# Kernel tuning notes

Measured on AMD Instinct MI355X. Metric: run time of the kernel, lower is better.

Reference implementation:

```python
import jax, jax.numpy as jnp
import numpy as np

N = 100000
E = 1000000
IN_C, HID, OUT_C = 128, 128, 40
DROPOUT_P = 0.5
BN_EPS = 1e-5


def setup_inputs() -> dict:
    key = jax.random.key(0)
    ks = jax.random.split(key, 10)
    x = jax.random.normal(ks[0], (N, IN_C), dtype=jnp.float32)
    edge_index = jax.random.randint(ks[1], (2, E), 0, N, dtype=jnp.int32)

    def glorot(k, fan_in, fan_out):
        lim = np.sqrt(6.0 / (fan_in + fan_out)).astype(np.float32)
        return jax.random.uniform(k, (fan_in, fan_out), jnp.float32, -lim, lim)

    return {
        "x": x,
        "edge_index": edge_index,
        "W1": glorot(ks[2], IN_C, HID), "b1": jnp.zeros((HID,), jnp.float32),
        "g1": jnp.ones((HID,), jnp.float32), "be1": jnp.zeros((HID,), jnp.float32),
        "W2": glorot(ks[3], HID, HID), "b2": jnp.zeros((HID,), jnp.float32),
        "g2": jnp.ones((HID,), jnp.float32), "be2": jnp.zeros((HID,), jnp.float32),
        "W3": glorot(ks[4], HID, OUT_C), "b3": jnp.zeros((OUT_C,), jnp.float32),
    }


def _deg_inv_sqrt(dst):
    # degree from destination nodes, +1 for the added self loop (PyG gcn_norm)
    deg = jax.ops.segment_sum(jnp.ones((E,), jnp.float32), dst, num_segments=N) + 1.0
    return jax.lax.rsqrt(deg)


def _gcn_conv(h, W, b, src, dst, dinv):
    # h: [N, Cin] -> [N, Cout]; y = D^-1/2 (A + I) D^-1/2 (h W) + b
    hw = h @ W
    norm = dinv[src] * dinv[dst]                      # [E]
    msg = hw[src] * norm[:, None]                     # [E, Cout] gather (memory-bound)
    agg = jax.ops.segment_sum(msg, dst, num_segments=N)
    agg = agg + hw * (dinv * dinv)[:, None]           # self-loop contribution
    return agg + b


def _batchnorm(h, gamma, beta):
    mu = jnp.mean(h, axis=0)
    var = jnp.mean(jnp.square(h - mu), axis=0)        # biased, training mode
    return (h - mu) * jax.lax.rsqrt(var + BN_EPS) * gamma + beta


def _dropout(h, key):
    keep = jax.random.bernoulli(key, 1.0 - DROPOUT_P, h.shape)
    return jnp.where(keep, h / (1.0 - DROPOUT_P), 0.0)


def reference(x, edge_index, W1, b1, g1, be1, W2, b2, g2, be2, W3, b3):
    src, dst = edge_index[0], edge_index[1]
    dinv = _deg_inv_sqrt(dst)
    dk = jax.random.split(jax.random.key(42), 2)

    h = _gcn_conv(x, W1, b1, src, dst, dinv)
    h = _dropout(jax.nn.relu(_batchnorm(h, g1, be1)), dk[0])

    h = _gcn_conv(h, W2, b2, src, dst, dinv)
    h = _dropout(jax.nn.relu(_batchnorm(h, g2, be2)), dk[1])

    h = _gcn_conv(h, W3, b3, src, dst, dinv)
    return jax.nn.log_softmax(h, axis=1)
```

## Files before the change

### kernel.cpp

```cpp
#include <hip/hip_runtime.h>
#include <math.h>

typedef __attribute__((ext_vector_type(8))) short bf16x8;
typedef __attribute__((ext_vector_type(4))) float f32x4;

__device__ __forceinline__ float bfbits2f(unsigned short b){
  return __uint_as_float(((unsigned)b) << 16);
}
__device__ __forceinline__ unsigned short f2bfbits(float f){
  unsigned u = __float_as_uint(f);
  unsigned r = u + 0x7fffu + ((u >> 16) & 1u);
  return (unsigned short)(r >> 16);
}

__device__ __forceinline__ uint4 ld16(const void* __restrict__ base, unsigned byteoff){
  return *(const uint4*)((const char*)base + byteoff);
}
__device__ __forceinline__ uint2 ld8(const void* __restrict__ base, unsigned byteoff){
  return *(const uint2*)((const char*)base + byteoff);
}

__host__ __device__ __forceinline__ unsigned rotl32(unsigned v, int d){
  return (v << d) | (v >> (32 - d));
}
__host__ __device__ __forceinline__ void tf2x32(unsigned k0, unsigned k1,
                                                unsigned c0, unsigned c1,
                                                unsigned &o0, unsigned &o1)
{
  unsigned ks2 = k0 ^ k1 ^ 0x1BD11BDAu;
  unsigned x0 = c0 + k0, x1 = c1 + k1;
#define TFR(r) x0 += x1; x1 = rotl32(x1, r); x1 ^= x0;
  TFR(13) TFR(15) TFR(26) TFR(6)
  x0 += k1;  x1 += ks2 + 1u;
  TFR(17) TFR(29) TFR(16) TFR(24)
  x0 += ks2; x1 += k0 + 2u;
  TFR(13) TFR(15) TFR(26) TFR(6)
  x0 += k0;  x1 += k1 + 3u;
  TFR(17) TFR(29) TFR(16) TFR(24)
  x0 += k1;  x1 += ks2 + 4u;
  TFR(13) TFR(15) TFR(26) TFR(6)
  x0 += ks2; x1 += k0 + 5u;
#undef TFR
  o0 = x0; o1 = x1;
}

__device__ __forceinline__ void gen_mask(unsigned* __restrict__ mask,
                                         unsigned mk0, unsigned mk1,
                                         int g, int total, int M)
{
  for (int wi = g; wi < M; wi += total){
    unsigned bits = 0u;
    #pragma unroll 4
    for (int j = 0; j < 32; j++){
      unsigned w0, w1;
      tf2x32(mk0, mk1, 0u, (unsigned)wi * 32u + (unsigned)j, w0, w1);
      bits |= (((w0 ^ w1) >> 31) << j);
    }
    mask[wi] = bits;
  }
}

__global__ __launch_bounds__(256) void k_countpos(const int* __restrict__ dst,
                                                  int* __restrict__ cnt,
                                                  int* __restrict__ pos, int E,
                                                  unsigned* __restrict__ mask,
                                                  unsigned mk0, unsigned mk1, int M)
{
  int g = blockIdx.x * 256 + threadIdx.x;
  int base = g * 4;
  if (base + 3 < E){
    int4 d = ((const int4*)dst)[g];
    int4 p;
    p.x = atomicAdd(&cnt[d.x], 1);
    p.y = atomicAdd(&cnt[d.y], 1);
    p.z = atomicAdd(&cnt[d.z], 1);
    p.w = atomicAdd(&cnt[d.w], 1);
    gen_mask(mask, mk0, mk1, g, gridDim.x * 256, M);
    ((int4*)pos)[g] = p;
  } else {
    for (int j = 0; j < 4; j++){
      int e = base + j;
      if (e < E) pos[e] = atomicAdd(&cnt[dst[e]], 1);
    }
    gen_mask(mask, mk0, mk1, g, gridDim.x * 256, M);
  }
}

__global__ __launch_bounds__(256) void k_blocksum(const int* __restrict__ cnt,
                                                  int* __restrict__ bsum, int N)
{
  __shared__ int sh[256];
  int t = threadIdx.x;
  int base = blockIdx.x * 1024 + t * 4;
  int s = 0;
  #pragma unroll
  for (int j = 0; j < 4; j++){ int i = base + j; if (i < N) s += cnt[i]; }
  sh[t] = s; __syncthreads();
  for (int off = 128; off; off >>= 1){
    if (t < off) sh[t] += sh[t + off];
    __syncthreads();
  }
  if (t == 0) bsum[blockIdx.x] = sh[0];
}

__global__ __launch_bounds__(256) void k_scansums(const int* __restrict__ bsum,
                                                  int* __restrict__ boff,
                                                  int* __restrict__ rowstart,
                                                  int NB, int N)
{
  __shared__ int sh[256];
  int t = threadIdx.x;
  int v = (t < NB) ? bsum[t] : 0;
  sh[t] = v; __syncthreads();
  for (int off = 1; off < 256; off <<= 1){
    int x = sh[t];
    int y = (t >= off) ? sh[t - off] : 0;
    __syncthreads();
    sh[t] = x + y;
    __syncthreads();
  }
  if (t < NB) boff[t] = sh[t] - v;
  if (t == NB - 1) rowstart[N] = sh[t];
}

__global__ __launch_bounds__(256) void k_scanfinal(const int* __restrict__ cnt,
                                                   const int* __restrict__ boff,
                                                   int* __restrict__ rowstart,
                                                   float* __restrict__ dinv, int N)
{
  __shared__ int sh[256];
  int t = threadIdx.x;
  int base = blockIdx.x * 1024 + t * 4;
  int c0 = 0, c1 = 0, c2 = 0, c3 = 0;
  if (base + 0 < N) c0 = cnt[base + 0];
  if (base + 1 < N) c1 = cnt[base + 1];
  if (base + 2 < N) c2 = cnt[base + 2];
  if (base + 3 < N) c3 = cnt[base + 3];
  int s = c0 + c1 + c2 + c3;
  sh[t] = s; __syncthreads();
  for (int off = 1; off < 256; off <<= 1){
    int x = sh[t];
    int y = (t >= off) ? sh[t - off] : 0;
    __syncthreads();
    sh[t] = x + y;
    __syncthreads();
  }
  int excl = sh[t] - s + boff[blockIdx.x];
  if (base + 0 < N){ rowstart[base+0] = excl;          dinv[base+0] = rsqrtf((float)c0 + 1.f); }
  if (base + 1 < N){ rowstart[base+1] = excl+c0;       dinv[base+1] = rsqrtf((float)c1 + 1.f); }
  if (base + 2 < N){ rowstart[base+2] = excl+c0+c1;    dinv[base+2] = rsqrtf((float)c2 + 1.f); }
  if (base + 3 < N){ rowstart[base+3] = excl+c0+c1+c2; dinv[base+3] = rsqrtf((float)c3 + 1.f); }
}

__global__ __launch_bounds__(256) void k_fill(const int* __restrict__ src,
                                              const int* __restrict__ dst,
                                              const int* __restrict__ pos,
                                              const int* __restrict__ rowstart,
                                              int* __restrict__ csr, int E,
                                              unsigned* __restrict__ mask,
                                              unsigned mk0, unsigned mk1, int M)
{
  int g = blockIdx.x * 256 + threadIdx.x;
  int base = g * 4;
  if (base + 3 < E){
    int4 d = ((const int4*)dst)[g];
    int4 p = ((const int4*)pos)[g];
    int4 s = ((const int4*)src)[g];
    int r0 = rowstart[d.x], r1 = rowstart[d.y], r2 = rowstart[d.z], r3 = rowstart[d.w];
    csr[r0 + p.x] = s.x;
    csr[r1 + p.y] = s.y;
    csr[r2 + p.z] = s.z;
    csr[r3 + p.w] = s.w;
  } else {
    for (int j = 0; j < 4; j++){
      int e = base + j;
      if (e < E) csr[rowstart[dst[e]] + pos[e]] = src[e];
    }
  }
  gen_mask(mask, mk0, mk1, g, gridDim.x * 256, M);
}

__global__ __launch_bounds__(256) void k_wt(const float* __restrict__ W1,
                                            const float* __restrict__ W2,
                                            const float* __restrict__ W3,
                                            unsigned short* __restrict__ WT1,
                                            unsigned short* __restrict__ WT2,
                                            unsigned short* __restrict__ WT3)
{
  const float* W; unsigned short* WT; int Cout, Cpad;
  if (blockIdx.x == 0){ W = W1; WT = WT1; Cout = 128; Cpad = 128; }
  else if (blockIdx.x == 1){ W = W2; WT = WT2; Cout = 128; Cpad = 128; }
  else { W = W3; WT = WT3; Cout = 40; Cpad = 48; }
  int tot = Cpad * 128;
  for (int i = threadIdx.x; i < tot; i += 256){
    int n = i >> 7, k = i & 127;
    float v = (n < Cout) ? W[k * Cout + n] : 0.f;
    WT[i] = f2bfbits(v);
  }
}

template<int NT, int MODE>
__global__ __launch_bounds__(256) void k_gemm_mfma(const void* __restrict__ Ap,
                                                   const unsigned short* __restrict__ WT,
                                                   const float* __restrict__ dinv,
                                                   const float* __restrict__ stats,
                                                   const float* __restrict__ g,
                                                   const float* __restrict__ be,
                                                   const unsigned* __restrict__ mask,
                                                   float invN,
                                                   unsigned short* __restrict__ outb,
                                                   int N, int Cout, int Cstride)
{
  __shared__ uint4 Wl4[NT * 16 * 16];
  __shared__ uint4 Al4[64 * 16];
  __shared__ float bnS[128], bnB[128];
  const int t = threadIdx.x;
  const int w = t >> 6, l = t & 63;
  const long rb0 = (long)blockIdx.x * 64;
  const int wrow0 = w * 16;

  uint4 rawU[4];
  float4 rawF[4][2];
  unsigned mword[4];
  int rr[4], cc[4];
  bool inr[4];
  #pragma unroll
  for (int i = 0; i < 4; i++){
    int idx = i * 64 + l;
    int r = idx >> 4, c = idx & 15;
    long grow = rb0 + wrow0 + r;
    rr[i] = r; cc[i] = c; inr[i] = (grow < N);
    if (inr[i]){
      if (MODE == 0){
        const float* ap = (const float*)Ap + grow * 128 + c * 8;
        rawF[i][0] = *(const float4*)ap;
        rawF[i][1] = *(const float4*)(ap + 4);
      } else {
        rawU[i] = *(const uint4*)((const unsigned short*)Ap + grow * 128 + c * 8);
        mword[i] = mask[((unsigned)grow << 2) + (c >> 2)];
      }
    }
  }

  {
    const uint4* s4 = (const uint4*)WT;
    const int tot = NT * 16 * 16;
    for (int i = t; i < tot; i += 256){
      int n = i >> 4, c = i & 15;
      Wl4[n * 16 + (c ^ (n & 15))] = s4[i];
    }
  }
  if (MODE == 2 && t < 128){
    float ss = 0.f, qq = 0.f;
    #pragma unroll
    for (int i = 0; i < 16; i++){
      ss += stats[i * 256 + t];
      qq += stats[i * 256 + 128 + t];
    }
    float mean = ss * invN;
    float var = fmaxf(qq * invN - mean * mean, 0.f);
    float rstd = rsqrtf(var + 1e-5f);
    float sc = g[t] * rstd;
    bnS[t] = sc;
    bnB[t] = be[t] - mean * sc;
  }
  __syncthreads();

  #pragma unroll
  for (int i = 0; i < 4; i++){
    uint4 chunk = make_uint4(0u, 0u, 0u, 0u);
    if (inr[i]){
      if (MODE == 0){
        chunk.x = (unsigned)f2bfbits(rawF[i][0].x) | ((unsigned)f2bfbits(rawF[i][0].y) << 16);
        chunk.y = (unsigned)f2bfbits(rawF[i][0].z) | ((unsigned)f2bfbits(rawF[i][0].w) << 16);
        chunk.z = (unsigned)f2bfbits(rawF[i][1].x) | ((unsigned)f2bfbits(rawF[i][1].y) << 16);
        chunk.w = (unsigned)f2bfbits(rawF[i][1].z) | ((unsigned)f2bfbits(rawF[i][1].w) << 16);
      } else {
        unsigned mb = mword[i] >> ((cc[i] & 3) * 8);
        const unsigned* rw = &rawU[i].x;
        unsigned* cw = &chunk.x;
        #pragma unroll
        for (int h = 0; h < 4; h++){
          int ch = cc[i] * 8 + 2 * h;
          float f0 = bfbits2f((unsigned short)(rw[h] & 0xffffu));
          float f1 = bfbits2f((unsigned short)(rw[h] >> 16));
          f0 = fmaxf(fmaf(f0, bnS[ch],     bnB[ch]),     0.f);
          f1 = fmaxf(fmaf(f1, bnS[ch + 1], bnB[ch + 1]), 0.f);
          f0 = ((mb >> (2 * h))     & 1u) ? 0.f : f0 * 2.f;
          f1 = ((mb >> (2 * h + 1)) & 1u) ? 0.f : f1 * 2.f;
          cw[h] = (unsigned)f2bfbits(f0) | ((unsigned)f2bfbits(f1) << 16);
        }
      }
    }
    Al4[(wrow0 + rr[i]) * 16 + (cc[i] ^ rr[i])] = chunk;
  }

  const int lm = l & 15, q = l >> 4;

  f32x4 acc[NT];
  #pragma unroll
  for (int nt = 0; nt < NT; nt++){
    acc[nt][0] = 0.f; acc[nt][1] = 0.f; acc[nt][2] = 0.f; acc[nt][3] = 0.f;
  }

  #pragma unroll
  for (int kt = 0; kt < 4; kt++){
    const int x = kt * 4 + q;
    bf16x8 a = *(const bf16x8*)&Al4[(wrow0 + lm) * 16 + (x ^ lm)];
    #pragma unroll
    for (int nt = 0; nt < NT; nt++){
      int brow = nt * 16 + lm;
      bf16x8 b = *(const bf16x8*)&Wl4[brow * 16 + (x ^ (brow & 15))];
      acc[nt] = __builtin_amdgcn_mfma_f32_16x16x32_bf16(a, b, acc[nt], 0, 0, 0);
    }
  }

  #pragma unroll
  for (int r = 0; r < 4; r++){
    long row = rb0 + wrow0 + q * 4 + r;
    if (row < N){
      float dv = dinv[row];
      #pragma unroll
      for (int nt = 0; nt < NT; nt++){
        int col = nt * 16 + lm;
        if (col < Cout)
          outb[row * Cstride + col] = f2bfbits(acc[nt][r] * dv);
      }
    }
  }
}

#define ACC8(U) do{ uint4 _u = (U); \
  a0 += bfbits2f((unsigned short)(_u.x & 0xffffu)); \
  a1 += bfbits2f((unsigned short)(_u.x >> 16)); \
  a2 += bfbits2f((unsigned short)(_u.y & 0xffffu)); \
  a3 += bfbits2f((unsigned short)(_u.y >> 16)); \
  a4 += bfbits2f((unsigned short)(_u.z & 0xffffu)); \
  a5 += bfbits2f((unsigned short)(_u.z >> 16)); \
  a6 += bfbits2f((unsigned short)(_u.w & 0xffffu)); \
  a7 += bfbits2f((unsigned short)(_u.w >> 16)); }while(0)

__global__ __launch_bounds__(256) void k_agg128s(const unsigned short* __restrict__ hw,
                                                 const int* __restrict__ rs,
                                                 const int* __restrict__ csr,
                                                 const float* __restrict__ dinv,
                                                 unsigned short* __restrict__ outb,
                                                 float* __restrict__ stats,
                                                 int N)
{
  const int l = threadIdx.x;
  const int ns = l >> 4;
  const int sl = l & 15;
  const int ty = threadIdx.y;
  const int grp = ty * 4 + ns;
  const int base = blockIdx.x * 32;
  const unsigned slB = (unsigned)sl * 16u;

  float s0=0.f,s1=0.f,s2=0.f,s3=0.f,s4=0.f,s5=0.f,s6=0.f,s7=0.f;
  float q0=0.f,q1=0.f,q2=0.f,q3=0.f,q4=0.f,q5=0.f,q6=0.f,q7=0.f;

  #pragma unroll 1
  for (int it = 0; it < 2; it++){
    int v = base + it * 16 + grp;
    if (v < N){
      float a0=0.f,a1=0.f,a2=0.f,a3=0.f,a4=0.f,a5=0.f,a6=0.f,a7=0.f;
      ACC8(ld16(hw, (unsigned)v * 256u + slB));
      int e0 = rs[v], e1 = rs[v + 1];
      int i = e0;
      for (; i + 4 <= e1; i += 4){
        int sa = csr[i], sb = csr[i+1], sc = csr[i+2], sd = csr[i+3];
        uint4 m0 = ld16(hw, (unsigned)sa * 256u + slB);
        uint4 m1 = ld16(hw, (unsigned)sb * 256u + slB);
        uint4 m2 = ld16(hw, (unsigned)sc * 256u + slB);
        uint4 m3 = ld16(hw, (unsigned)sd * 256u + slB);
        ACC8(m0); ACC8(m1); ACC8(m2); ACC8(m3);
      }
      for (; i < e1; i++){
        ACC8(ld16(hw, (unsigned)csr[i] * 256u + slB));
      }
      float dv = dinv[v];
      a0*=dv; a1*=dv; a2*=dv; a3*=dv; a4*=dv; a5*=dv; a6*=dv; a7*=dv;
      uint4 o;
      o.x = (unsigned)f2bfbits(a0) | ((unsigned)f2bfbits(a1) << 16);
      o.y = (unsigned)f2bfbits(a2) | ((unsigned)f2bfbits(a3) << 16);
      o.z = (unsigned)f2bfbits(a4) | ((unsigned)f2bfbits(a5) << 16);
      o.w = (unsigned)f2bfbits(a6) | ((unsigned)f2bfbits(a7) << 16);
      *(uint4*)((char*)outb + (unsigned)v * 256u + slB) = o;
      s0+=a0; q0=fmaf(a0,a0,q0);  s1+=a1; q1=fmaf(a1,a1,q1);
      s2+=a2; q2=fmaf(a2,a2,q2);  s3+=a3; q3=fmaf(a3,a3,q3);
      s4+=a4; q4=fmaf(a4,a4,q4);  s5+=a5; q5=fmaf(a5,a5,q5);
      s6+=a6; q6=fmaf(a6,a6,q6);  s7+=a7; q7=fmaf(a7,a7,q7);
    }
  }

  __shared__ float shS[16][128], shQ[16][128];
  *(float4*)&shS[grp][sl * 8]     = make_float4(s0, s1, s2, s3);
  *(float4*)&shS[grp][sl * 8 + 4] = make_float4(s4, s5, s6, s7);
  *(float4*)&shQ[grp][sl * 8]     = make_float4(q0, q1, q2, q3);
  *(float4*)&shQ[grp][sl * 8 + 4] = make_float4(q4, q5, q6, q7);
  __syncthreads();
  int t = ty * 64 + threadIdx.x;
  if (t < 128){
    float ss = 0.f, qq = 0.f;
    #pragma unroll
    for (int g2 = 0; g2 < 16; g2++){ ss += shS[g2][t]; qq += shQ[g2][t]; }
    float* dstat = stats + (blockIdx.x & 15) * 256;
    atomicAdd(&dstat[t], ss);
    atomicAdd(&dstat[128 + t], qq);
  }
}

__global__ __launch_bounds__(256) void k_agg40lsm(const unsigned short* __restrict__ hw,
                                                  const int* __restrict__ rs,
                                                  const int* __restrict__ csr,
                                                  const float* __restrict__ dinv,
                                                  const float* __restrict__ b3,
                                                  float* __restrict__ out, int N)
{
  const int l = threadIdx.x;
  const int ns = l >> 4, sl = l & 15;
  const int v = blockIdx.x * 16 + threadIdx.y * 4 + ns;
  const bool act = (v < N) && (sl < 10);
  const unsigned slB = (unsigned)sl * 8u;
  float a0 = 0.f, a1 = 0.f, a2 = 0.f, a3 = 0.f, dv = 1.f;
  if (act){
    dv = dinv[v];
    uint2 u = ld8(hw, (unsigned)v * 128u + slB);
    a0 = bfbits2f((unsigned short)(u.x & 0xffffu));
    a1 = bfbits2f((unsigned short)(u.x >> 16));
    a2 = bfbits2f((unsigned short)(u.y & 0xffffu));
    a3 = bfbits2f((unsigned short)(u.y >> 16));
    int e0 = rs[v], e1 = rs[v + 1];
    int i = e0;
#define ACCU2(U) do{ uint2 _u = (U); \
    a0 += bfbits2f((unsigned short)(_u.x & 0xffffu)); \
    a1 += bfbits2f((unsigned short)(_u.x >> 16)); \
    a2 += bfbits2f((unsigned short)(_u.y & 0xffffu)); \
    a3 += bfbits2f((unsigned short)(_u.y >> 16)); }while(0)
    for (; i + 4 <= e1; i += 4){
      int sa = csr[i], sb = csr[i+1], sc = csr[i+2], sd = csr[i+3];
      uint2 m0 = ld8(hw, (unsigned)sa * 128u + slB);
      uint2 m1 = ld8(hw, (unsigned)sb * 128u + slB);
      uint2 m2 = ld8(hw, (unsigned)sc * 128u + slB);
      uint2 m3 = ld8(hw, (unsigned)sd * 128u + slB);
      ACCU2(m0); ACCU2(m1); ACCU2(m2); ACCU2(m3);
    }
    for (; i < e1; i++){
      ACCU2(ld8(hw, (unsigned)csr[i] * 128u + slB));
    }
#undef ACCU2
  }
  float x0 = act ? fmaf(a0, dv, b3[sl * 4 + 0]) : -INFINITY;
  float x1 = act ? fmaf(a1, dv, b3[sl * 4 + 1]) : -INFINITY;
  float x2 = act ? fmaf(a2, dv, b3[sl * 4 + 2]) : -INFINITY;
  float x3 = act ? fmaf(a3, dv, b3[sl * 4 + 3]) : -INFINITY;
  float m = fmaxf(fmaxf(x0, x1), fmaxf(x2, x3));
  #pragma unroll
  for (int off = 8; off; off >>= 1) m = fmaxf(m, __shfl_xor(m, off, 16));
  float e = act ? (expf(x0 - m) + expf(x1 - m) + expf(x2 - m) + expf(x3 - m)) : 0.f;
  #pragma unroll
  for (int off = 8; off; off >>= 1) e += __shfl_xor(e, off, 16);
  float lse = m + logf(e);
  if (act){
    float4 o;
    o.x = x0 - lse; o.y = x1 - lse; o.z = x2 - lse; o.w = x3 - lse;
    *reinterpret_cast<float4*>(out + (size_t)v * 40 + sl * 4) = o;
  }
}

extern "C" void kernel_launch(void* const* d_in, const int* in_sizes, int n_in,
                              void* d_out, int out_size, void* d_ws, size_t ws_size,
                              hipStream_t stream)
{
  const float* x  = (const float*)d_in[0];
  const int* ei   = (const int*)d_in[1];
  const float* W1 = (const float*)d_in[2];
  const float* g1 = (const float*)d_in[4];
  const float* be1= (const float*)d_in[5];
  const float* W2 = (const float*)d_in[6];
  const float* g2 = (const float*)d_in[8];
  const float* be2= (const float*)d_in[9];
  const float* W3 = (const float*)d_in[10];
  const float* b3 = (const float*)d_in[11];
  float* out = (float*)d_out;

  const int N = in_sizes[0] / 128;
  const int E = in_sizes[1] / 2;
  const int* srcv = ei;
  const int* dstv = ei + E;

  char* ws = (char*)d_ws;
  size_t off = 0;
  auto take = [&](size_t bytes) -> void* {
    void* p = ws + off;
    off = (off + bytes + 255) & ~(size_t)255;
    return p;
  };
  int*   cnt      = (int*)  take((size_t)N * 4);
  int*   pos      = (int*)  take((size_t)E * 4);
  int*   rowstart = (int*)  take((size_t)(N + 1) * 4);
  int*   csr      = (int*)  take((size_t)E * 4);
  float* dinv     = (float*)take((size_t)N * 4);
  int*   bsum     = (int*)  take(256 * 4);
  int*   boff     = (int*)  take(256 * 4);
  float* stats1   = (float*)take(2 * 16 * 256 * 4);
  float* stats2   = stats1 + 16 * 256;
  unsigned* mask1 = (unsigned*)take((size_t)N * 4 * 4);
  unsigned* mask2 = (unsigned*)take((size_t)N * 4 * 4);
  unsigned short* WT1 = (unsigned short*)take(128 * 128 * 2);
  unsigned short* WT2 = (unsigned short*)take(128 * 128 * 2);
  unsigned short* WT3 = (unsigned short*)take(48 * 128 * 2);
  unsigned short* bufX = (unsigned short*)take((size_t)N * 128 * 2);
  unsigned short* bufY = (unsigned short*)take((size_t)N * 128 * 2);
  (void)ws_size; (void)n_in; (void)out_size;

  unsigned l1k0, l1k1, l2k0, l2k1;
  tf2x32(0u, 42u, 0u, 0u, l1k0, l1k1);
  tf2x32(0u, 42u, 0u, 1u, l2k0, l2k1);

  const float invN = 1.0f / (float)N;
  const int M = N * 4;
  const int NB = (N + 1023) / 1024;
  dim3 wblk(64, 4);
  dim3 wgrid16((N + 15) / 16);
  dim3 wgrid32((N + 31) / 32);
  const int ggrid = (N + 63) / 64;
  const int egrid = (E + 1023) / 1024;

  hipMemsetAsync(cnt, 0, (size_t)N * 4, stream);
  hipMemsetAsync(stats1, 0, 2 * 16 * 256 * 4, stream);
  k_countpos<<<egrid, 256, 0, stream>>>(dstv, cnt, pos, E, mask1, l1k0, l1k1, M);
  k_blocksum<<<NB, 256, 0, stream>>>(cnt, bsum, N);
  k_scansums<<<1, 256, 0, stream>>>(bsum, boff, rowstart, NB, N);
  k_scanfinal<<<NB, 256, 0, stream>>>(cnt, boff, rowstart, dinv, N);
  k_fill<<<egrid, 256, 0, stream>>>(srcv, dstv, pos, rowstart, csr, E, mask2, l2k0, l2k1, M);
  k_wt<<<3, 256, 0, stream>>>(W1, W2, W3, WT1, WT2, WT3);

  k_gemm_mfma<8, 0><<<ggrid, 256, 0, stream>>>(x, WT1, dinv,
      nullptr, nullptr, nullptr, nullptr, invN, bufX, N, 128, 128);
  k_agg128s<<<wgrid32, wblk, 0, stream>>>(bufX, rowstart, csr, dinv, bufY, stats1, N);

  k_gemm_mfma<8, 2><<<ggrid, 256, 0, stream>>>(bufY, WT2, dinv,
      stats1, g1, be1, mask1, invN, bufX, N, 128, 128);
  k_agg128s<<<wgrid32, wblk, 0, stream>>>(bufX, rowstart, csr, dinv, bufY, stats2, N);

  k_gemm_mfma<3, 2><<<ggrid, 256, 0, stream>>>(bufY, WT3, dinv,
      stats2, g2, be2, mask2, invN, bufX, N, 40, 64);
  k_agg40lsm<<<wgrid16, wblk, 0, stream>>>(bufX, rowstart, csr, dinv, b3, out, N);
}
```

Before: 409.4 us.

## Split dropout mask generation into its own kernel and simplify CSR fill

After: 482.2 us. 1.18x slower.

```diff
diff --git a/kernel.cpp b/kernel.cpp
--- a/kernel.cpp
+++ b/kernel.cpp
@@ -44,45 +44,38 @@
   o0 = x0; o1 = x1;
 }
 
-__device__ __forceinline__ void gen_mask(unsigned* __restrict__ mask,
-                                         unsigned mk0, unsigned mk1,
-                                         int g, int total, int M)
-{
-  for (int wi = g; wi < M; wi += total){
-    unsigned bits = 0u;
-    #pragma unroll 4
-    for (int j = 0; j < 32; j++){
-      unsigned w0, w1;
-      tf2x32(mk0, mk1, 0u, (unsigned)wi * 32u + (unsigned)j, w0, w1);
-      bits |= (((w0 ^ w1) >> 31) << j);
-    }
-    mask[wi] = bits;
-  }
-}
-
-__global__ __launch_bounds__(256) void k_countpos(const int* __restrict__ dst,
-                                                  int* __restrict__ cnt,
-                                                  int* __restrict__ pos, int E,
-                                                  unsigned* __restrict__ mask,
-                                                  unsigned mk0, unsigned mk1, int M)
+__global__ __launch_bounds__(256) void k_mask(unsigned* __restrict__ mask1,
+                                              unsigned* __restrict__ mask2,
+                                              unsigned a0, unsigned a1,
+                                              unsigned b0, unsigned b1, int M)
 {
   int g = blockIdx.x * 256 + threadIdx.x;
-  int base = g * 4;
-  if (base + 3 < E){
-    int4 d = ((const int4*)dst)[g];
-    int4 p;
-    p.x = atomicAdd(&cnt[d.x], 1);
-    p.y = atomicAdd(&cnt[d.y], 1);
-    p.z = atomicAdd(&cnt[d.z], 1);
-    p.w = atomicAdd(&cnt[d.w], 1);
-    gen_mask(mask, mk0, mk1, g, gridDim.x * 256, M);
-    ((int4*)pos)[g] = p;
-  } else {
-    for (int j = 0; j < 4; j++){
-      int e = base + j;
-      if (e < E) pos[e] = atomicAdd(&cnt[dst[e]], 1);
-    }
-    gen_mask(mask, mk0, mk1, g, gridDim.x * 256, M);
+  if (g >= 2 * M) return;
+  const bool second = g >= M;
+  unsigned wi = second ? (unsigned)(g - M) : (unsigned)g;
+  unsigned k0 = second ? b0 : a0;
+  unsigned k1 = second ? b1 : a1;
+  unsigned bits = 0u;
+  #pragma unroll 4
+  for (int j = 0; j < 32; j++){
+    unsigned w0, w1;
+    tf2x32(k0, k1, 0u, wi * 32u + (unsigned)j, w0, w1);
+    bits |= (((w0 ^ w1) >> 31) << j);
+  }
+  (second ? mask2 : mask1)[wi] = bits;
+}
+
+__global__ __launch_bounds__(256) void k_count(const int* __restrict__ dst,
+                                               int* __restrict__ cnt, int E)
+{
+  int g = blockIdx.x * 256 + threadIdx.x;
+  int base = g * 2;
+  if (base + 1 < E){
+    int2 d = ((const int2*)dst)[g];
+    atomicAdd(&cnt[d.x], 1);
+    atomicAdd(&cnt[d.y], 1);
+  } else if (base < E){
+    atomicAdd(&cnt[dst[base]], 1);
   }
 }
 
@@ -123,7 +116,7 @@
   if (t == NB - 1) rowstart[N] = sh[t];
 }
 
-__global__ __launch_bounds__(256) void k_scanfinal(const int* __restrict__ cnt,
+__global__ __launch_bounds__(256) void k_scanfinal(int* __restrict__ cnt,
                                                    const int* __restrict__ boff,
                                                    int* __restrict__ rowstart,
                                                    float* __restrict__ dinv, int N)
@@ -146,38 +139,30 @@
     __syncthreads();
   }
   int excl = sh[t] - s + boff[blockIdx.x];
-  if (base + 0 < N){ rowstart[base+0] = excl;          dinv[base+0] = rsqrtf((float)c0 + 1.f); }
-  if (base + 1 < N){ rowstart[base+1] = excl+c0;       dinv[base+1] = rsqrtf((float)c1 + 1.f); }
-  if (base + 2 < N){ rowstart[base+2] = excl+c0+c1;    dinv[base+2] = rsqrtf((float)c2 + 1.f); }
-  if (base + 3 < N){ rowstart[base+3] = excl+c0+c1+c2; dinv[base+3] = rsqrtf((float)c3 + 1.f); }
+  if (base + 0 < N){ rowstart[base+0] = excl;          cnt[base+0] = excl;          dinv[base+0] = rsqrtf((float)c0 + 1.f); }
+  if (base + 1 < N){ rowstart[base+1] = excl+c0;       cnt[base+1] = excl+c0;       dinv[base+1] = rsqrtf((float)c1 + 1.f); }
+  if (base + 2 < N){ rowstart[base+2] = excl+c0+c1;    cnt[base+2] = excl+c0+c1;    dinv[base+2] = rsqrtf((float)c2 + 1.f); }
+  if (base + 3 < N){ rowstart[base+3] = excl+c0+c1+c2; cnt[base+3] = excl+c0+c1+c2; dinv[base+3] = rsqrtf((float)c3 + 1.f); }
 }
 
 __global__ __launch_bounds__(256) void k_fill(const int* __restrict__ src,
                                               const int* __restrict__ dst,
-                                              const int* __restrict__ pos,
-                                              const int* __restrict__ rowstart,
-                                              int* __restrict__ csr, int E,
-                                              unsigned* __restrict__ mask,
-                                              unsigned mk0, unsigned mk1, int M)
+                                              int* __restrict__ cur,
+                                              int* __restrict__ csr, int E)
 {
   int g = blockIdx.x * 256 + threadIdx.x;
-  int base = g * 4;
-  if (base + 3 < E){
-    int4 d = ((const int4*)dst)[g];
-    int4 p = ((const int4*)pos)[g];
-    int4 s = ((const int4*)src)[g];
-    int r0 = rowstart[d.x], r1 = rowstart[d.y], r2 = rowstart[d.z], r3 = rowstart[d.w];
-    csr[r0 + p.x] = s.x;
-    csr[r1 + p.y] = s.y;
-    csr[r2 + p.z] = s.z;
-    csr[r3 + p.w] = s.w;
-  } else {
-    for (int j = 0; j < 4; j++){
-      int e = base + j;
-      if (e < E) csr[rowstart[dst[e]] + pos[e]] = src[e];
-    }
-  }
-  gen_mask(mask, mk0, mk1, g, gridDim.x * 256, M);
+  int base = g * 2;
+  if (base + 1 < E){
+    int2 d = ((const int2*)dst)[g];
+    int2 s = ((const int2*)src)[g];
+    int p0 = atomicAdd(&cur[d.x], 1);
+    int p1 = atomicAdd(&cur[d.y], 1);
+    csr[p0] = s.x;
+    csr[p1] = s.y;
+  } else if (base < E){
+    int p0 = atomicAdd(&cur[dst[base]], 1);
+    csr[p0] = src[base];
+  }
 }
 
 __global__ __launch_bounds__(256) void k_wt(const float* __restrict__ W1,
@@ -497,7 +482,6 @@
     return p;
   };
   int*   cnt      = (int*)  take((size_t)N * 4);
-  int*   pos      = (int*)  take((size_t)E * 4);
   int*   rowstart = (int*)  take((size_t)(N + 1) * 4);
   int*   csr      = (int*)  take((size_t)E * 4);
   float* dinv     = (float*)take((size_t)N * 4);
@@ -525,16 +509,18 @@
   dim3 wgrid16((N + 15) / 16);
   dim3 wgrid32((N + 31) / 32);
   const int ggrid = (N + 63) / 64;
-  const int egrid = (E + 1023) / 1024;
+  const int e2grid = (E + 511) / 512;
+  const int mgrid = (2 * M + 255) / 256;
 
   hipMemsetAsync(cnt, 0, (size_t)N * 4, stream);
   hipMemsetAsync(stats1, 0, 2 * 16 * 256 * 4, stream);
-  k_countpos<<<egrid, 256, 0, stream>>>(dstv, cnt, pos, E, mask1, l1k0, l1k1, M);
+  k_count<<<e2grid, 256, 0, stream>>>(dstv, cnt, E);
   k_blocksum<<<NB, 256, 0, stream>>>(cnt, bsum, N);
   k_scansums<<<1, 256, 0, stream>>>(bsum, boff, rowstart, NB, N);
   k_scanfinal<<<NB, 256, 0, stream>>>(cnt, boff, rowstart, dinv, N);
-  k_fill<<<egrid, 256, 0, stream>>>(srcv, dstv, pos, rowstart, csr, E, mask2, l2k0, l2k1, M);
+  k_fill<<<e2grid, 256, 0, stream>>>(srcv, dstv, cnt, csr, E);
   k_wt<<<3, 256, 0, stream>>>(W1, W2, W3, WT1, WT2, WT3);
+  k_mask<<<mgrid, 256, 0, stream>>>(mask1, mask2, l1k0, l1k1, l2k0, l2k1, M);
 
   k_gemm_mfma<8, 0><<<ggrid, 256, 0, stream>>>(x, WT1, dinv,
       nullptr, nullptr, nullptr, nullptr, invN, bufX, N, 128, 128);
```

## Slice GEMM output into 16-channel column planes for cache-local aggregation, move mask gen

Applied to the files above, without the earlier changes.

Result: slower. 524.3 us (+28.1%).

```diff
diff --git a/kernel.cpp b/kernel.cpp
--- a/kernel.cpp
+++ b/kernel.cpp
@@ -3,6 +3,7 @@
 
 typedef __attribute__((ext_vector_type(8))) short bf16x8;
 typedef __attribute__((ext_vector_type(4))) float f32x4;
+typedef __attribute__((ext_vector_type(4))) unsigned uint32x4;
 
 __device__ __forceinline__ float bfbits2f(unsigned short b){
   return __uint_as_float(((unsigned)b) << 16);
@@ -44,27 +45,9 @@
   o0 = x0; o1 = x1;
 }
 
-__device__ __forceinline__ void gen_mask(unsigned* __restrict__ mask,
-                                         unsigned mk0, unsigned mk1,
-                                         int g, int total, int M)
-{
-  for (int wi = g; wi < M; wi += total){
-    unsigned bits = 0u;
-    #pragma unroll 4
-    for (int j = 0; j < 32; j++){
-      unsigned w0, w1;
-      tf2x32(mk0, mk1, 0u, (unsigned)wi * 32u + (unsigned)j, w0, w1);
-      bits |= (((w0 ^ w1) >> 31) << j);
-    }
-    mask[wi] = bits;
-  }
-}
-
 __global__ __launch_bounds__(256) void k_countpos(const int* __restrict__ dst,
                                                   int* __restrict__ cnt,
-                                                  int* __restrict__ pos, int E,
-                                                  unsigned* __restrict__ mask,
-                                                  unsigned mk0, unsigned mk1, int M)
+                                                  int* __restrict__ pos, int E)
 {
   int g = blockIdx.x * 256 + threadIdx.x;
   int base = g * 4;
@@ -75,14 +58,12 @@
     p.y = atomicAdd(&cnt[d.y], 1);
     p.z = atomicAdd(&cnt[d.z], 1);
     p.w = atomicAdd(&cnt[d.w], 1);
-    gen_mask(mask, mk0, mk1, g, gridDim.x * 256, M);
     ((int4*)pos)[g] = p;
   } else {
     for (int j = 0; j < 4; j++){
       int e = base + j;
       if (e < E) pos[e] = atomicAdd(&cnt[dst[e]], 1);
     }
-    gen_mask(mask, mk0, mk1, g, gridDim.x * 256, M);
   }
 }
 
@@ -156,9 +137,7 @@
                                               const int* __restrict__ dst,
                                               const int* __restrict__ pos,
                                               const int* __restrict__ rowstart,
-                                              int* __restrict__ csr, int E,
-                                              unsigned* __restrict__ mask,
-                                              unsigned mk0, unsigned mk1, int M)
+                                              int* __restrict__ csr, int E)
 {
   int g = blockIdx.x * 256 + threadIdx.x;
   int base = g * 4;
@@ -177,7 +156,6 @@
       if (e < E) csr[rowstart[dst[e]] + pos[e]] = src[e];
     }
   }
-  gen_mask(mask, mk0, mk1, g, gridDim.x * 256, M);
 }
 
 __global__ __launch_bounds__(256) void k_wt(const float* __restrict__ W1,
@@ -199,7 +177,7 @@
   }
 }
 
-template<int NT, int MODE>
+template<int NT, int MODE, int SPLITOUT, int MASKGEN>
 __global__ __launch_bounds__(256) void k_gemm_mfma(const void* __restrict__ Ap,
                                                    const unsigned short* __restrict__ WT,
                                                    const float* __restrict__ dinv,
@@ -207,6 +185,8 @@
                                                    const float* __restrict__ g,
                                                    const float* __restrict__ be,
                                                    const unsigned* __restrict__ mask,
+                                                   unsigned* __restrict__ maskw,
+                                                   unsigned wk0, unsigned wk1, int Mw,
                                                    float invN,
                                                    unsigned short* __restrict__ outb,
                                                    int N, int Cout, int Cstride)
@@ -323,14 +303,33 @@
       #pragma unroll
       for (int nt = 0; nt < NT; nt++){
         int col = nt * 16 + lm;
-        if (col < Cout)
-          outb[row * Cstride + col] = f2bfbits(acc[nt][r] * dv);
-      }
-    }
-  }
-}
-
-#define ACC8(U) do{ uint4 _u = (U); \
+        if (SPLITOUT){
+          unsigned slice = (unsigned)col >> 4, wi = (unsigned)col & 15;
+          outb[((size_t)slice * N + row) * 16 + wi] = f2bfbits(acc[nt][r] * dv);
+        } else {
+          if (col < Cout)
+            outb[row * Cstride + col] = f2bfbits(acc[nt][r] * dv);
+        }
+      }
+    }
+  }
+
+  if (MASKGEN){
+    int gg = blockIdx.x * 256 + t;
+    if (gg < Mw){
+      unsigned bits = 0u;
+      #pragma unroll 4
+      for (int j = 0; j < 32; j++){
+        unsigned w0, w1;
+        tf2x32(wk0, wk1, 0u, (unsigned)gg * 32u + (unsigned)j, w0, w1);
+        bits |= (((w0 ^ w1) >> 31) << j);
+      }
+      maskw[gg] = bits;
+    }
+  }
+}
+
+#define ACC8U(U) do{ uint4 _u = (U); \
   a0 += bfbits2f((unsigned short)(_u.x & 0xffffu)); \
   a1 += bfbits2f((unsigned short)(_u.x >> 16)); \
   a2 += bfbits2f((unsigned short)(_u.y & 0xffffu)); \
@@ -340,52 +339,68 @@
   a6 += bfbits2f((unsigned short)(_u.w & 0xffffu)); \
   a7 += bfbits2f((unsigned short)(_u.w >> 16)); }while(0)
 
-__global__ __launch_bounds__(256) void k_agg128s(const unsigned short* __restrict__ hw,
-                                                 const int* __restrict__ rs,
-                                                 const int* __restrict__ csr,
-                                                 const float* __restrict__ dinv,
-                                                 unsigned short* __restrict__ outb,
-                                                 float* __restrict__ stats,
-                                                 int N)
+__global__ __launch_bounds__(256) void k_agg128sp(const unsigned short* __restrict__ hw,
+                                                  const int* __restrict__ rs,
+                                                  const int* __restrict__ csr,
+                                                  const float* __restrict__ dinv,
+                                                  unsigned short* __restrict__ outb,
+                                                  float* __restrict__ stats,
+                                                  int N)
 {
   const int l = threadIdx.x;
-  const int ns = l >> 4;
-  const int sl = l & 15;
   const int ty = threadIdx.y;
-  const int grp = ty * 4 + ns;
-  const int base = blockIdx.x * 32;
-  const unsigned slB = (unsigned)sl * 16u;
+  const int slice = blockIdx.x & 7;
+  const int nb = blockIdx.x >> 3;
+  const int grp = ty * 32 + (l >> 1);
+  const int sub = l & 1;
+  const unsigned sliceB = (unsigned)slice * (unsigned)N * 32u;
+  const unsigned subB = (unsigned)sub * 16u;
+  const unsigned outO = (unsigned)slice * 32u + subB;
 
   float s0=0.f,s1=0.f,s2=0.f,s3=0.f,s4=0.f,s5=0.f,s6=0.f,s7=0.f;
   float q0=0.f,q1=0.f,q2=0.f,q3=0.f,q4=0.f,q5=0.f,q6=0.f,q7=0.f;
 
   #pragma unroll 1
   for (int it = 0; it < 2; it++){
-    int v = base + it * 16 + grp;
+    int v = nb * 256 + it * 128 + grp;
     if (v < N){
-      float a0=0.f,a1=0.f,a2=0.f,a3=0.f,a4=0.f,a5=0.f,a6=0.f,a7=0.f;
-      ACC8(ld16(hw, (unsigned)v * 256u + slB));
+      float a0,a1,a2,a3,a4,a5,a6,a7;
+      {
+        uint4 u = ld16(hw, sliceB + (unsigned)v * 32u + subB);
+        a0 = bfbits2f((unsigned short)(u.x & 0xffffu));
+        a1 = bfbits2f((unsigned short)(u.x >> 16));
+        a2 = bfbits2f((unsigned short)(u.y & 0xffffu));
+        a3 = bfbits2f((unsigned short)(u.y >> 16));
+        a4 = bfbits2f((unsigned short)(u.z & 0xffffu));
+        a5 = bfbits2f((unsigned short)(u.z >> 16));
+        a6 = bfbits2f((unsigned short)(u.w & 0xffffu));
+        a7 = bfbits2f((unsigned short)(u.w >> 16));
+      }
       int e0 = rs[v], e1 = rs[v + 1];
       int i = e0;
       for (; i + 4 <= e1; i += 4){
-        int sa = csr[i], sb = csr[i+1], sc = csr[i+2], sd = csr[i+3];
-        uint4 m0 = ld16(hw, (unsigned)sa * 256u + slB);
-        uint4 m1 = ld16(hw, (unsigned)sb * 256u + slB);
-        uint4 m2 = ld16(hw, (unsigned)sc * 256u + slB);
-        uint4 m3 = ld16(hw, (unsigned)sd * 256u + slB);
-        ACC8(m0); ACC8(m1); ACC8(m2); ACC8(m3);
+        int sa = __builtin_nontemporal_load(csr + i);
+        int sb = __builtin_nontemporal_load(csr + i + 1);
+        int sc = __builtin_nontemporal_load(csr + i + 2);
+        int sd = __builtin_nontemporal_load(csr + i + 3);
+        uint4 m0 = ld16(hw, sliceB + (unsigned)sa * 32u + subB);
+        uint4 m1 = ld16(hw, sliceB + (unsigned)sb * 32u + subB);
+        uint4 m2 = ld16(hw, sliceB + (unsigned)sc * 32u + subB);
+        uint4 m3 = ld16(hw, sliceB + (unsigned)sd * 32u + subB);
+        ACC8U(m0); ACC8U(m1); ACC8U(m2); ACC8U(m3);
       }
       for (; i < e1; i++){
-        ACC8(ld16(hw, (unsigned)csr[i] * 256u + slB));
+        int sa = __builtin_nontemporal_load(csr + i);
+        ACC8U(ld16(hw, sliceB + (unsigned)sa * 32u + subB));
       }
       float dv = dinv[v];
       a0*=dv; a1*=dv; a2*=dv; a3*=dv; a4*=dv; a5*=dv; a6*=dv; a7*=dv;
-      uint4 o;
+      uint32x4 o;
       o.x = (unsigned)f2bfbits(a0) | ((unsigned)f2bfbits(a1) << 16);
       o.y = (unsigned)f2bfbits(a2) | ((unsigned)f2bfbits(a3) << 16);
       o.z = (unsigned)f2bfbits(a4) | ((unsigned)f2bfbits(a5) << 16);
       o.w = (unsigned)f2bfbits(a6) | ((unsigned)f2bfbits(a7) << 16);
-      *(uint4*)((char*)outb + (unsigned)v * 256u + slB) = o;
+      __builtin_nontemporal_store(o, (uint32x4*)((char*)outb + (unsigned)v * 256u + outO));
       s0+=a0; q0=fmaf(a0,a0,q0);  s1+=a1; q1=fmaf(a1,a1,q1);
       s2+=a2; q2=fmaf(a2,a2,q2);  s3+=a3; q3=fmaf(a3,a3,q3);
       s4+=a4; q4=fmaf(a4,a4,q4);  s5+=a5; q5=fmaf(a5,a5,q5);
@@ -393,20 +408,31 @@
     }
   }
 
-  __shared__ float shS[16][128], shQ[16][128];
-  *(float4*)&shS[grp][sl * 8]     = make_float4(s0, s1, s2, s3);
-  *(float4*)&shS[grp][sl * 8 + 4] = make_float4(s4, s5, s6, s7);
-  *(float4*)&shQ[grp][sl * 8]     = make_float4(q0, q1, q2, q3);
-  *(float4*)&shQ[grp][sl * 8 + 4] = make_float4(q4, q5, q6, q7);
+  __shared__ float shS[128][17], shQ[128][17];
+  int cb = sub * 8;
+  shS[grp][cb+0]=s0; shS[grp][cb+1]=s1; shS[grp][cb+2]=s2; shS[grp][cb+3]=s3;
+  shS[grp][cb+4]=s4; shS[grp][cb+5]=s5; shS[grp][cb+6]=s6; shS[grp][cb+7]=s7;
+  shQ[grp][cb+0]=q0; shQ[grp][cb+1]=q1; shQ[grp][cb+2]=q2; shQ[grp][cb+3]=q3;
+  shQ[grp][cb+4]=q4; shQ[grp][cb+5]=q5; shQ[grp][cb+6]=q6; shQ[grp][cb+7]=q7;
   __syncthreads();
-  int t = ty * 64 + threadIdx.x;
-  if (t < 128){
+  int t = ty * 64 + l;
+  int ch = t & 15, part = t >> 4;
+  float ps = 0.f, pq = 0.f;
+  #pragma unroll
+  for (int k = 0; k < 8; k++){
+    ps += shS[part * 8 + k][ch];
+    pq += shQ[part * 8 + k][ch];
+  }
+  __shared__ float s2m[16][17], q2m[16][17];
+  s2m[part][ch] = ps; q2m[part][ch] = pq;
+  __syncthreads();
+  if (t < 16){
     float ss = 0.f, qq = 0.f;
     #pragma unroll
-    for (int g2 = 0; g2 < 16; g2++){ ss += shS[g2][t]; qq += shQ[g2][t]; }
+    for (int p = 0; p < 16; p++){ ss += s2m[p][t]; qq += q2m[p][t]; }
     float* dstat = stats + (blockIdx.x & 15) * 256;
-    atomicAdd(&dstat[t], ss);
-    atomicAdd(&dstat[128 + t], qq);
+    atomicAdd(&dstat[slice * 16 + t], ss);
+    atomicAdd(&dstat[128 + slice * 16 + t], qq);
   }
 }
 
@@ -523,28 +549,31 @@
   const int NB = (N + 1023) / 1024;
   dim3 wblk(64, 4);
   dim3 wgrid16((N + 15) / 16);
-  dim3 wgrid32((N + 31) / 32);
+  const int sgrid = 8 * ((N + 255) / 256);
   const int ggrid = (N + 63) / 64;
   const int egrid = (E + 1023) / 1024;
 
   hipMemsetAsync(cnt, 0, (size_t)N * 4, stream);
   hipMemsetAsync(stats1, 0, 2 * 16 * 256 * 4, stream);
-  k_countpos<<<egrid, 256, 0, stream>>>(dstv, cnt, pos, E, mask1, l1k0, l1k1, M);
+  k_countpos<<<egrid, 256, 0, stream>>>(dstv, cnt, pos, E);
   k_blocksum<<<NB, 256, 0, stream>>>(cnt, bsum, N);
   k_scansums<<<1, 256, 0, stream>>>(bsum, boff, rowstart, NB, N);
   k_scanfinal<<<NB, 256, 0, stream>>>(cnt, boff, rowstart, dinv, N);
-  k_fill<<<egrid, 256, 0, stream>>>(srcv, dstv, pos, rowstart, csr, E, mask2, l2k0, l2k1, M);
+  k_fill<<<egrid, 256, 0, stream>>>(srcv, dstv, pos, rowstart, csr, E);
   k_wt<<<3, 256, 0, stream>>>(W1, W2, W3, WT1, WT2, WT3);
 
-  k_gemm_mfma<8, 0><<<ggrid, 256, 0, stream>>>(x, WT1, dinv,
-      nullptr, nullptr, nullptr, nullptr, invN, bufX, N, 128, 128);
-  k_agg128s<<<wgrid32, wblk, 0, stream>>>(bufX, rowstart, csr, dinv, bufY, stats1, N);
-
-  k_gemm_mfma<8, 2><<<ggrid, 256, 0, stream>>>(bufY, WT2, dinv,
-      stats1, g1, be1, mask1, invN, bufX, N, 128, 128);
-  k_agg128s<<<wgrid32, wblk, 0, stream>>>(bufX, rowstart, csr, dinv, bufY, stats2, N);
-
-  k_gemm_mfma<3, 2><<<ggrid, 256, 0, stream>>>(bufY, WT3, dinv,
-      stats2, g2, be2, mask2, invN, bufX, N, 40, 64);
+  k_gemm_mfma<8, 0, 1, 1><<<ggrid, 256, 0, stream>>>(x, WT1, dinv,
+      nullptr, nullptr, nullptr, nullptr, mask1, l1k0, l1k1, M,
+      invN, bufX, N, 128, 128);
+  k_agg128sp<<<sgrid, wblk, 0, stream>>>(bufX, rowstart, csr, dinv, bufY, stats1, N);
+
+  k_gemm_mfma<8, 2, 1, 1><<<ggrid, 256, 0, stream>>>(bufY, WT2, dinv,
+      stats1, g1, be1, mask1, mask2, l2k0, l2k1, M,
+      invN, bufX, N, 128, 128);
+  k_agg128sp<<<sgrid, wblk, 0, stream>>>(bufX, rowstart, csr, dinv, bufY, stats2, N);
+
+  k_gemm_mfma<3, 2, 0, 0><<<ggrid, 256, 0, stream>>>(bufY, WT3, dinv,
+      stats2, g2, be2, mask2, nullptr, 0u, 0u, 0,
+      invN, bufX, N, 40, 64);
   k_agg40lsm<<<wgrid16, wblk, 0, stream>>>(bufX, rowstart, csr, dinv, b3, out, N);
 }
```
